# Performance work log

Measured on AMD Instinct MI355X. Metric: run time of the kernel, lower is better.

The kernel has to match this reference:

```python
import jax, jax.numpy as jnp
import numpy as np


def fwht(x):
    """Unnormalized fast Walsh-Hadamard transform over a 1-D vector (len = power of 2).
    Matches the torch chunk/cat stage ordering (MSB-first butterfly)."""
    n = x.shape[0]
    ll = int(round(np.log2(n)))
    for ii in range(ll):
        x = x.reshape(2 ** ii, 2, -1)
        x = jnp.concatenate([x[:, :1] + x[:, 1:], x[:, :1] - x[:, 1:]], axis=1)
    return x.reshape(n)


@jax.custom_vjp
def fwht_ff(x):
    # mirrors torch FastWalshHadamard.apply: plain FWHT forward,
    # backward = FWHT(grad) / sqrt(n) (as defined in the original autograd Function)
    return fwht(x)

def _fwht_ff_fwd(x):
    scale = jnp.asarray(1.0 / np.sqrt(float(x.shape[0])), x.dtype)
    return fwht(x), scale

def _fwht_ff_bwd(scale, g):
    return (scale * fwht(g),)

fwht_ff.defvjp(_fwht_ff_fwd, _fwht_ff_bwd)


def fastfood(theta, BB, Pi, GG, DD):
    """Fastfood projection of theta (dim dd) to DD dims using fixed vars."""
    LL = BB.shape[0]
    dd = theta.shape[0]
    k = min(dd, LL)  # F.pad with negative pad truncates; replicate that
    xx = jnp.zeros(LL, theta.dtype).at[:k].set(theta[:k])
    m2 = fwht(BB * xx)          # H B x
    m4 = m2[Pi] * GG            # G Pi H B x
    m5 = fwht_ff(m4)            # H G Pi H B x
    divisor = jnp.sqrt(LL * jnp.sum(GG * GG))
    return m5[:DD] / (divisor * np.sqrt(float(DD) / LL))


def _mk_ff_vars(key, DD):
    ll = int(np.ceil(np.log2(DD)))
    LL = 2 ** ll
    k1, k2, k3 = jax.random.split(key, 3)
    BB = jax.random.randint(k1, (LL,), 0, 2).astype(jnp.float32) * 2.0 - 1.0
    Pi = jax.random.permutation(k2, LL).astype(jnp.int32)
    GG = jax.random.normal(k3, (LL,), dtype=jnp.float32)
    return BB, Pi, GG


D_IN, D_HID, D_OUT = 768, 3072, 768
INTRINSIC = 2048
BATCH = 256


def setup_inputs() -> dict:
    key = jax.random.key(0)
    ks = jax.random.split(key, 12)
    x = jax.random.normal(ks[0], (BATCH, D_IN), dtype=jnp.float32)
    # original initializes intrinsic_parameter to zeros; use small randn so the
    # Fastfood path contributes non-trivially to the output for testing
    theta = jax.random.normal(ks[1], (INTRINSIC,), dtype=jnp.float32) * 0.01
    init_W1 = jax.random.normal(ks[2], (D_HID, D_IN), dtype=jnp.float32) * 0.02
    init_b1 = jax.random.normal(ks[3], (D_HID,), dtype=jnp.float32) * 0.02
    init_W2 = jax.random.normal(ks[4], (D_OUT, D_HID), dtype=jnp.float32) * 0.02
    init_b2 = jax.random.normal(ks[5], (D_OUT,), dtype=jnp.float32) * 0.02
    BB_W1, Pi_W1, GG_W1 = _mk_ff_vars(ks[6], D_HID * D_IN)
    BB_b1, Pi_b1, GG_b1 = _mk_ff_vars(ks[7], D_HID)
    BB_W2, Pi_W2, GG_W2 = _mk_ff_vars(ks[8], D_OUT * D_HID)
    BB_b2, Pi_b2, GG_b2 = _mk_ff_vars(ks[9], D_OUT)
    return {
        'x': x, 'theta': theta,
        'init_W1': init_W1, 'init_b1': init_b1, 'init_W2': init_W2, 'init_b2': init_b2,
        'BB_W1': BB_W1, 'Pi_W1': Pi_W1, 'GG_W1': GG_W1,
        'BB_b1': BB_b1, 'Pi_b1': Pi_b1, 'GG_b1': GG_b1,
        'BB_W2': BB_W2, 'Pi_W2': Pi_W2, 'GG_W2': GG_W2,
        'BB_b2': BB_b2, 'Pi_b2': Pi_b2, 'GG_b2': GG_b2,
    }


def reference(x, theta, init_W1, init_b1, init_W2, init_b2,
              BB_W1, Pi_W1, GG_W1, BB_b1, Pi_b1, GG_b1,
              BB_W2, Pi_W2, GG_W2, BB_b2, Pi_b2, GG_b2):
    # param = initial_value + fastfood(theta) for every wrapped parameter
    W1 = init_W1 + fastfood(theta, BB_W1, Pi_W1, GG_W1, init_W1.size).reshape(init_W1.shape)
    b1 = init_b1 + fastfood(theta, BB_b1, Pi_b1, GG_b1, init_b1.size)
    W2 = init_W2 + fastfood(theta, BB_W2, Pi_W2, GG_W2, init_W2.size).reshape(init_W2.shape)
    b2 = init_b2 + fastfood(theta, BB_b2, Pi_b2, GG_b2, init_b2.size)
    # wrapped module forward: Linear -> ReLU -> Linear
    h = jax.nn.relu(x @ W1.T + b1)
    return h @ W2.T + b2
```

## Files before the change

### kernel.cpp

```cpp
#include <hip/hip_runtime.h>
#include <hip/hip_bf16.h>

typedef __attribute__((ext_vector_type(8))) short bf16x8;
typedef __attribute__((ext_vector_type(8))) unsigned short u16x8;
typedef __attribute__((ext_vector_type(4))) float f32x4;

#define LLW 4194304

template <int N, int S>
__device__ __forceinline__ void reg_fwht(float* v) {
#pragma unroll
  for (int h = 1; h < N; h <<= 1)
#pragma unroll
    for (int g = 0; g < N; g += 2 * h)
#pragma unroll
      for (int j = 0; j < h; ++j) {
        float a = v[(g + j) * S], b = v[(g + j + h) * S];
        v[(g + j) * S] = a + b;
        v[(g + j + h) * S] = a - b;
      }
}

__device__ __forceinline__ unsigned short f2bf(float f) {
  unsigned u = __float_as_uint(f);
  unsigned r = (u + 0x7fff + ((u >> 16) & 1)) >> 16;
  return (unsigned short)r;
}

__device__ __forceinline__ void lds_fwht(float* s, int n, int tid, int T) {
  for (int h = 1; h < n; h <<= 1) {
    __syncthreads();
    for (int t = tid; t < (n >> 1); t += T) {
      int i0 = ((t & ~(h - 1)) << 1) | (t & (h - 1));
      int i1 = i0 + h;
      float a = s[i0], b = s[i1];
      s[i0] = a + b;
      s[i1] = a - b;
    }
  }
  __syncthreads();
}

__device__ __forceinline__ void fwht2048_block(float w[8], float* pad,
                                               float* dst, int t) {
  reg_fwht<8, 1>(w);
#pragma unroll
  for (int j = 0; j < 8; ++j) {
    int i = t + 256 * j;
    pad[i + 4 * (i >> 5)] = w[j];
  }
  __syncthreads();
  {
    int base = 8 * t + 4 * (t >> 2);
    float4 a = *(float4*)(pad + base);
    float4 b = *(float4*)(pad + base + 4);
    float u[8] = {a.x, a.y, a.z, a.w, b.x, b.y, b.z, b.w};
    reg_fwht<8, 1>(u);
    *(float4*)(pad + base) = make_float4(u[0], u[1], u[2], u[3]);
    *(float4*)(pad + base + 4) = make_float4(u[4], u[5], u[6], u[7]);
  }
  __syncthreads();
  {
    int b0 = (t & 7) + 64 * (t >> 3);
    float u[8];
#pragma unroll
    for (int j = 0; j < 8; ++j) {
      int i = b0 + 8 * j;
      u[j] = pad[i + 4 * (i >> 5)];
    }
    reg_fwht<8, 1>(u);
#pragma unroll
    for (int j = 0; j < 8; ++j) {
      int i = b0 + 8 * j;
      pad[i + 4 * (i >> 5)] = u[j];
    }
  }
  __syncthreads();
#pragma unroll
  for (int g = 0; g < 2; ++g) {
    int b0 = (t & 63) + 256 * ((g << 2) | (t >> 6));
    float u[4];
#pragma unroll
    for (int j = 0; j < 4; ++j) {
      int i = b0 + 64 * j;
      u[j] = pad[i + 4 * (i >> 5)];
    }
    reg_fwht<4, 1>(u);
#pragma unroll
    for (int j = 0; j < 4; ++j) dst[b0 + 64 * j] = u[j];
  }
  __syncthreads();
}

__global__ __launch_bounds__(256, 4) void k_front(
    const float* __restrict__ BB1, const int* __restrict__ Pi1,
    const float* __restrict__ GG1, const float* __restrict__ BB2,
    const int* __restrict__ Pi2, const float* __restrict__ GG2,
    unsigned short* __restrict__ m4b, float* __restrict__ partial,
    const float* __restrict__ theta, const float* __restrict__ BBb1,
    const int* __restrict__ Pib1, const float* __restrict__ GGb1,
    const float* __restrict__ ib1, float* __restrict__ b1w,
    const float* __restrict__ BBb2, const int* __restrict__ Pib2,
    const float* __restrict__ GGb2, const float* __restrict__ ib2,
    float* __restrict__ b2w, const float* __restrict__ x,
    __hip_bfloat16* __restrict__ xb) {
  __shared__ __align__(16) float s[9216];
  __shared__ float red[4];
  int b = blockIdx.x, t = threadIdx.x;

  if (b >= 98) {
    int job = b - 98;
    int pipe = job >> 9, chunk = job & 511;
    const float* BB = pipe ? BB2 : BB1;
    const int* Pi = pipe ? Pi2 : Pi1;
    const float* GG = pipe ? GG2 : GG1;

    long base = (long)chunk * 8192;
    const int4* p4 = (const int4*)(Pi + base);
    const float4* g4 = (const float4*)(GG + base);
    int4 pp[8];
    float4 gg[8];
#pragma unroll
    for (int j = 0; j < 8; ++j) {
      pp[j] = p4[t + j * 256];
      gg[j] = g4[t + j * 256];
    }

    {
      float w8[8];
#pragma unroll
      for (int j = 0; j < 8; ++j) {
        int i = t + 256 * j;
        w8[j] = BB[i] * theta[i];
      }
      fwht2048_block(w8, s + 2304, s, t);
    }

    float v[32];
    float lsum = 0.f;
#pragma unroll
    for (int j = 0; j < 8; ++j) {
      lsum += gg[j].x * gg[j].x + gg[j].y * gg[j].y + gg[j].z * gg[j].z +
              gg[j].w * gg[j].w;
      v[j * 4 + 0] = s[pp[j].x & 2047] * gg[j].x;
      v[j * 4 + 1] = s[pp[j].y & 2047] * gg[j].y;
      v[j * 4 + 2] = s[pp[j].z & 2047] * gg[j].z;
      v[j * 4 + 3] = s[pp[j].w & 2047] * gg[j].w;
    }
    for (int off = 32; off; off >>= 1) lsum += __shfl_down(lsum, off, 64);
    if ((t & 63) == 0) red[t >> 6] = lsum;

#pragma unroll
    for (int e = 0; e < 4; ++e) reg_fwht<8, 4>(v + e);

    __syncthreads();
    if (t == 0)
      partial[pipe * 512 + chunk] = red[0] + red[1] + red[2] + red[3];

#pragma unroll
    for (int j = 0; j < 8; ++j) {
      int A = t * 4 + 4 * (t >> 3) + j * 1152;
      *(float4*)(s + A) =
          make_float4(v[j * 4], v[j * 4 + 1], v[j * 4 + 2], v[j * 4 + 3]);
    }
    __syncthreads();
    {
      int b0 = (t & 31) + (t >> 5) * 1024;
      float w[32];
#pragma unroll
      for (int j2 = 0; j2 < 32; ++j2) {
        int i = b0 + j2 * 32;
        w[j2] = s[i + 4 * (i >> 5)];
      }
      reg_fwht<32, 1>(w);
#pragma unroll
      for (int j2 = 0; j2 < 32; ++j2) {
        int i = b0 + j2 * 32;
        s[i + 4 * (i >> 5)] = w[j2];
      }
    }
    __syncthreads();
#pragma unroll
    for (int q = 0; q < 8; ++q) {
      float4 r = *(const float4*)(s + t * 36 + q * 4);
      v[q * 4 + 0] = r.x;
      v[q * 4 + 1] = r.y;
      v[q * 4 + 2] = r.z;
      v[q * 4 + 3] = r.w;
    }
    reg_fwht<32, 1>(v);
    unsigned short* o = m4b + (long)pipe * LLW;
    long a0 = (long)(2 * t) * 8192 + (long)chunk * 16;
#pragma unroll
    for (int q = 0; q < 4; ++q) {
      u16x8 pk;
#pragma unroll
      for (int e = 0; e < 8; ++e) pk[e] = f2bf(v[q * 8 + e]);
      *(u16x8*)(o + a0 + (q >> 1) * 8192 + (q & 1) * 8) = pk;
    }
  } else if (b < 96) {
    int id0 = b * 256 + t;
#pragma unroll
    for (int it = 0; it < 2; ++it) {
      int id = id0 + it * 24576;
      float4 xv = ((const float4*)x)[id];
      ushort4 o;
      o.x = f2bf(xv.x);
      o.y = f2bf(xv.y);
      o.z = f2bf(xv.z);
      o.w = f2bf(xv.w);
      ((ushort4*)xb)[id] = o;
    }
  } else if (b == 96) {
    float* tabd = s + 6144;
    float w[8];
#pragma unroll
    for (int j = 0; j < 8; ++j) {
      int i = t + 256 * j;
      w[j] = BBb1[i] * theta[i];
    }
    fwht2048_block(w, s, tabd, t);

    float w16[16];
    float lsum = 0.f;
#pragma unroll
    for (int j = 0; j < 16; ++j) {
      int i = t + 256 * j;
      float g = GGb1[i];
      lsum += g * g;
      w16[j] = tabd[Pib1[i] & 2047] * g;
    }
    reg_fwht<16, 1>(w16);
#pragma unroll
    for (int j = 0; j < 16; ++j) {
      int i = t + 256 * j;
      s[i + 4 * (i >> 5)] = w16[j];
    }
    for (int off = 32; off; off >>= 1) lsum += __shfl_down(lsum, off, 64);
    if ((t & 63) == 0) s[4608 + (t >> 6)] = lsum;
    __syncthreads();
    float S = s[4608] + s[4609] + s[4610] + s[4611];
    {
      int base16 = 16 * t + 4 * (t >> 1);
      float u[16];
#pragma unroll
      for (int q = 0; q < 4; ++q) {
        float4 r = *(float4*)(s + base16 + q * 4);
        u[q * 4 + 0] = r.x;
        u[q * 4 + 1] = r.y;
        u[q * 4 + 2] = r.z;
        u[q * 4 + 3] = r.w;
      }
      reg_fwht<16, 1>(u);
#pragma unroll
      for (int q = 0; q < 4; ++q)
        *(float4*)(s + base16 + q * 4) =
            make_float4(u[q * 4], u[q * 4 + 1], u[q * 4 + 2], u[q * 4 + 3]);
    }
    __syncthreads();
    {
      float scale = 1.0f / sqrtf(S * 3072.0f);
      int b0 = (t & 15) + 256 * (t >> 4);
      float u[16];
#pragma unroll
      for (int j = 0; j < 16; ++j) {
        int i = b0 + 16 * j;
        u[j] = s[i + 4 * (i >> 5)];
      }
      reg_fwht<16, 1>(u);
#pragma unroll
      for (int j = 0; j < 16; ++j) {
        int i = b0 + 16 * j;
        if (i < 3072) b1w[i] = ib1[i] + u[j] * scale;
      }
    }
  } else {
    float* tab2 = s;
    float* m42 = s + 1024;
    for (int i = t; i < 1024; i += 256) tab2[i] = BBb2[i] * theta[i];
    lds_fwht(tab2, 1024, t, 256);
    float lsum = 0.f;
    for (int i = t; i < 1024; i += 256) {
      float g = GGb2[i];
      lsum += g * g;
      m42[i] = tab2[Pib2[i] & 1023] * g;
    }
    for (int off = 32; off; off >>= 1) lsum += __shfl_down(lsum, off, 64);
    if ((t & 63) == 0) s[2048 + (t >> 6)] = lsum;
    lds_fwht(m42, 1024, t, 256);
    float S = s[2048] + s[2049] + s[2050] + s[2051];
    float scale = 1.0f / sqrtf(S * 768.0f);
    for (int i = t; i < 768; i += 256) b2w[i] = ib2[i] + m42[i] * scale;
  }
}

__global__ __launch_bounds__(256) void k_f2c(
    const unsigned short* __restrict__ m4b, const float* __restrict__ iW1,
    const float* __restrict__ iW2, const float* __restrict__ partial,
    __hip_bfloat16* __restrict__ W1b, __hip_bfloat16* __restrict__ W2b) {
  __shared__ __align__(16) float s[10480];
  __shared__ float red[4];
  int b = blockIdx.x, t = threadIdx.x;
  int pipe = b >> 9;
  int lb = b & 511;
  int g = ((lb & 7) << 6) | (lb >> 3);
  int l0 = g * 16;
  const unsigned short* mp = m4b + (long)pipe * LLW + (long)g * 8192;
  const float* initW = pipe ? iW2 : iW1;
  unsigned short* outW = (unsigned short*)(pipe ? W2b : W1b);

  float4 ivp[5];
#pragma unroll
  for (int u = 0; u < 5; ++u) {
    int idx = t + u * 256;
    if (idx < 1152) {
      int r = idx >> 2, c4 = (idx & 3) * 4;
      ivp[u] = *(const float4*)(initW + (long)r * 8192 + l0 + c4);
    }
  }

  {
    float ps = partial[pipe * 512 + t] + partial[pipe * 512 + 256 + t];
    for (int off = 32; off; off >>= 1) ps += __shfl_down(ps, off, 64);
    if ((t & 63) == 0) red[t >> 6] = ps;
  }

#pragma unroll
  for (int q = 0; q < 4; ++q) {
    u16x8 raw = *(const u16x8*)(mp + t * 32 + q * 8);
    int r = 2 * t + (q >> 1), cb = (q & 1) * 8;
    float* dp = s + r * 20 + (r >> 5) * 16 + cb;
    float4 f0, f1v;
    f0.x = __uint_as_float((unsigned)raw[0] << 16);
    f0.y = __uint_as_float((unsigned)raw[1] << 16);
    f0.z = __uint_as_float((unsigned)raw[2] << 16);
    f0.w = __uint_as_float((unsigned)raw[3] << 16);
    f1v.x = __uint_as_float((unsigned)raw[4] << 16);
    f1v.y = __uint_as_float((unsigned)raw[5] << 16);
    f1v.z = __uint_as_float((unsigned)raw[6] << 16);
    f1v.w = __uint_as_float((unsigned)raw[7] << 16);
    *(float4*)dp = f0;
    *(float4*)(dp + 4) = f1v;
  }
  __syncthreads();

  {
    int c = t & 15, rg = t >> 4;
    float w[32];
#pragma unroll
    for (int j = 0; j < 32; ++j) {
      int r = rg * 32 + j;
      w[j] = s[r * 20 + (r >> 5) * 16 + c];
    }
    reg_fwht<32, 1>(w);
#pragma unroll
    for (int j = 0; j < 32; ++j) {
      int r = rg * 32 + j;
      s[r * 20 + (r >> 5) * 16 + c] = w[j];
    }
  }
  __syncthreads();

  {
    int c = t & 15;
    float w[32];
#pragma unroll
    for (int k = 0; k < 2; ++k) {
      int b0 = (t >> 4) * 2 + k;
#pragma unroll
      for (int j4 = 0; j4 < 16; ++j4) {
        int r = b0 + 32 * j4;
        w[k * 16 + j4] = s[r * 20 + (r >> 5) * 16 + c];
      }
      reg_fwht<16, 1>(w + k * 16);
#pragma unroll
      for (int j4 = 0; j4 < 16; ++j4) {
        int r = b0 + 32 * j4;
        s[r * 20 + (r >> 5) * 16 + c] = w[k * 16 + j4];
      }
    }
  }
  __syncthreads();

  float S = red[0] + red[1] + red[2] + red[3];
  float scale = 1.0f / sqrtf(S * 2359296.0f);
#pragma unroll
  for (int u = 0; u < 5; ++u) {
    int idx = t + u * 256;
    if (idx < 1152) {
      int r = idx >> 2, c4 = (idx & 3) * 4;
      const float* sp = s + r * 20 + (r >> 5) * 16 + c4;
      long gi = (long)r * 8192 + l0 + c4;
      ushort4 pk;
      pk.x = f2bf(ivp[u].x + sp[0] * scale);
      pk.y = f2bf(ivp[u].y + sp[1] * scale);
      pk.z = f2bf(ivp[u].z + sp[2] * scale);
      pk.w = f2bf(ivp[u].w + sp[3] * scale);
      *(ushort4*)(outW + gi) = pk;
    }
  }
}

template <int NACC, int SPLITK, bool RELU, bool OUT_BF16>
__global__ __launch_bounds__(256) void k_gemm(
    const __hip_bfloat16* __restrict__ A, const __hip_bfloat16* __restrict__ B,
    const float* __restrict__ bias, void* __restrict__ C, int M, int N, int K) {
  __shared__ float red[4 * NACC * 320];
  int wave = threadIdx.x >> 6, lane = threadIdx.x & 63;
  int tileid = blockIdx.x * (4 / SPLITK) + wave / SPLITK;
  int sk = wave % SPLITK;
  int ntiles = N / (16 * NACC);
  int mt = tileid / ntiles, nt = tileid % ntiles;
  int ml = lane & 15;
  int q = lane >> 4;
  const short* As = (const short*)A;
  const short* Bs = (const short*)B;
  long arow = (long)(mt * 16 + ml) * K + q * 8;
  int KS = K / SPLITK, k0 = sk * KS;
  f32x4 acc[NACC] = {};
  for (int k = k0; k < k0 + KS; k += 32) {
    bf16x8 av = *(const bf16x8*)(As + arow + k);
#pragma unroll
    for (int a = 0; a < NACC; ++a) {
      int n = nt * 16 * NACC + a * 16 + ml;
      bf16x8 bv = *(const bf16x8*)(Bs + (long)n * K + q * 8 + k);
      acc[a] = __builtin_amdgcn_mfma_f32_16x16x32_bf16(av, bv, acc[a], 0, 0, 0);
    }
  }
#pragma unroll
  for (int a = 0; a < NACC; ++a)
#pragma unroll
    for (int r = 0; r < 4; ++r)
      red[(wave * NACC + a) * 320 + lane * 5 + r] = acc[a][r];
  __syncthreads();
  if (sk == 0) {
#pragma unroll
    for (int a = 0; a < NACC; ++a) {
      int n = nt * 16 * NACC + a * 16 + ml;
      float bv = bias[n];
#pragma unroll
      for (int r = 0; r < 4; ++r) {
        float vv = bv;
#pragma unroll
        for (int j = 0; j < SPLITK; ++j)
          vv += red[((wave + j) * NACC + a) * 320 + lane * 5 + r];
        int mm = mt * 16 + q * 4 + r;
        if (RELU) vv = fmaxf(vv, 0.f);
        if (OUT_BF16)
          ((__hip_bfloat16*)C)[(long)mm * N + n] = __float2bfloat16(vv);
        else
          ((float*)C)[(long)mm * N + n] = vv;
      }
    }
  }
}

#define OFF_PART 0
#define OFF_M2S 4096
#define OFF_M4B (OFF_M2S + 16384)
#define OFF_W1B (OFF_M4B + 2 * LLW * 2)
#define OFF_W2B (OFF_W1B + 4718592)
#define OFF_HB (OFF_W2B + 4718592)
#define OFF_XB (OFF_HB + 1572864)
#define OFF_B1 (OFF_XB + 393216)
#define OFF_B2 (OFF_B1 + 12288)

extern "C" void kernel_launch(void* const* d_in, const int* in_sizes, int n_in,
                              void* d_out, int out_size, void* d_ws,
                              size_t ws_size, hipStream_t stream) {
  const float* x = (const float*)d_in[0];
  const float* theta = (const float*)d_in[1];
  const float* iW1 = (const float*)d_in[2];
  const float* ib1 = (const float*)d_in[3];
  const float* iW2 = (const float*)d_in[4];
  const float* ib2 = (const float*)d_in[5];
  const float* BB_W1 = (const float*)d_in[6];
  const int* Pi_W1 = (const int*)d_in[7];
  const float* GG_W1 = (const float*)d_in[8];
  const float* BB_b1 = (const float*)d_in[9];
  const int* Pi_b1 = (const int*)d_in[10];
  const float* GG_b1 = (const float*)d_in[11];
  const float* BB_W2 = (const float*)d_in[12];
  const int* Pi_W2 = (const int*)d_in[13];
  const float* GG_W2 = (const float*)d_in[14];
  const float* BB_b2 = (const float*)d_in[15];
  const int* Pi_b2 = (const int*)d_in[16];
  const float* GG_b2 = (const float*)d_in[17];

  char* ws = (char*)d_ws;
  float* partial = (float*)(ws + OFF_PART);
  unsigned short* m4b = (unsigned short*)(ws + OFF_M4B);
  __hip_bfloat16* W1b = (__hip_bfloat16*)(ws + OFF_W1B);
  __hip_bfloat16* W2b = (__hip_bfloat16*)(ws + OFF_W2B);
  __hip_bfloat16* hb = (__hip_bfloat16*)(ws + OFF_HB);
  __hip_bfloat16* xb = (__hip_bfloat16*)(ws + OFF_XB);
  float* b1w = (float*)(ws + OFF_B1);
  float* b2w = (float*)(ws + OFF_B2);

  k_front<<<1122, 256, 0, stream>>>(BB_W1, Pi_W1, GG_W1, BB_W2, Pi_W2, GG_W2,
                                    m4b, partial, theta, BB_b1, Pi_b1, GG_b1,
                                    ib1, b1w, BB_b2, Pi_b2, GG_b2, ib2, b2w, x,
                                    xb);
  k_f2c<<<1024, 256, 0, stream>>>(m4b, iW1, iW2, partial, W1b, W2b);
  k_gemm<2, 2, true, true><<<768, 256, 0, stream>>>(xb, W1b, b1w, hb, 256,
                                                    3072, 768);
  k_gemm<1, 4, false, false><<<768, 256, 0, stream>>>(hb, W2b, b2w, d_out, 256,
                                                      768, 3072);
}
```

Baseline: 215.3 us.

## Run front Fastfood kernel with 512-thread blocks and re-stage 8192-point FWHT

Raises the k_front block size from 256 to 512 threads. Each thread now holds 16 elements of the 8192-point transform instead of 32. The transform after the permutation is rebuilt as a 4-point register stage, two 16-point LDS stages and an 8-point stage fused into the bf16 store. The aim is to cut register pressure and raise occupancy and parallelism per chunk. In exchange, the 2048-point theta transform uses only half the threads, and the deeper staging adds an extra LDS round trip and barrier.

```diff
diff --git a/kernel.cpp b/kernel.cpp
--- a/kernel.cpp
+++ b/kernel.cpp
@@ -41,16 +41,18 @@
   __syncthreads();
 }
 
-__device__ __forceinline__ void fwht2048_block(float w[8], float* pad,
-                                               float* dst, int t) {
-  reg_fwht<8, 1>(w);
-#pragma unroll
-  for (int j = 0; j < 8; ++j) {
-    int i = t + 256 * j;
-    pad[i + 4 * (i >> 5)] = w[j];
-  }
-  __syncthreads();
-  {
+__device__ __forceinline__ void fwht2048_block_g(float w[8], float* pad,
+                                                 float* dst, int t, bool act) {
+  if (act) {
+    reg_fwht<8, 1>(w);
+#pragma unroll
+    for (int j = 0; j < 8; ++j) {
+      int i = t + 256 * j;
+      pad[i + 4 * (i >> 5)] = w[j];
+    }
+  }
+  __syncthreads();
+  if (act) {
     int base = 8 * t + 4 * (t >> 2);
     float4 a = *(float4*)(pad + base);
     float4 b = *(float4*)(pad + base + 4);
@@ -60,7 +62,7 @@
     *(float4*)(pad + base + 4) = make_float4(u[4], u[5], u[6], u[7]);
   }
   __syncthreads();
-  {
+  if (act) {
     int b0 = (t & 7) + 64 * (t >> 3);
     float u[8];
 #pragma unroll
@@ -76,23 +78,25 @@
     }
   }
   __syncthreads();
-#pragma unroll
-  for (int g = 0; g < 2; ++g) {
-    int b0 = (t & 63) + 256 * ((g << 2) | (t >> 6));
-    float u[4];
-#pragma unroll
-    for (int j = 0; j < 4; ++j) {
-      int i = b0 + 64 * j;
-      u[j] = pad[i + 4 * (i >> 5)];
-    }
-    reg_fwht<4, 1>(u);
-#pragma unroll
-    for (int j = 0; j < 4; ++j) dst[b0 + 64 * j] = u[j];
-  }
-  __syncthreads();
-}
-
-__global__ __launch_bounds__(256, 4) void k_front(
+  if (act) {
+#pragma unroll
+    for (int g = 0; g < 2; ++g) {
+      int b0 = (t & 63) + 256 * ((g << 2) | (t >> 6));
+      float u[4];
+#pragma unroll
+      for (int j = 0; j < 4; ++j) {
+        int i = b0 + 64 * j;
+        u[j] = pad[i + 4 * (i >> 5)];
+      }
+      reg_fwht<4, 1>(u);
+#pragma unroll
+      for (int j = 0; j < 4; ++j) dst[b0 + 64 * j] = u[j];
+    }
+  }
+  __syncthreads();
+}
+
+__global__ __launch_bounds__(512, 6) void k_front(
     const float* __restrict__ BB1, const int* __restrict__ Pi1,
     const float* __restrict__ GG1, const float* __restrict__ BB2,
     const int* __restrict__ Pi2, const float* __restrict__ GG2,
@@ -105,7 +109,7 @@
     float* __restrict__ b2w, const float* __restrict__ x,
     __hip_bfloat16* __restrict__ xb) {
   __shared__ __align__(16) float s[9216];
-  __shared__ float red[4];
+  __shared__ float red[8];
   int b = blockIdx.x, t = threadIdx.x;
 
   if (b >= 98) {
@@ -118,28 +122,31 @@
     long base = (long)chunk * 8192;
     const int4* p4 = (const int4*)(Pi + base);
     const float4* g4 = (const float4*)(GG + base);
-    int4 pp[8];
-    float4 gg[8];
-#pragma unroll
-    for (int j = 0; j < 8; ++j) {
-      pp[j] = p4[t + j * 256];
-      gg[j] = g4[t + j * 256];
+    int4 pp[4];
+    float4 gg[4];
+#pragma unroll
+    for (int j = 0; j < 4; ++j) {
+      pp[j] = p4[t + j * 512];
+      gg[j] = g4[t + j * 512];
     }
 
     {
+      bool act = t < 256;
       float w8[8];
-#pragma unroll
-      for (int j = 0; j < 8; ++j) {
-        int i = t + 256 * j;
-        w8[j] = BB[i] * theta[i];
-      }
-      fwht2048_block(w8, s + 2304, s, t);
-    }
-
-    float v[32];
+      if (act) {
+#pragma unroll
+        for (int j = 0; j < 8; ++j) {
+          int i = t + 256 * j;
+          w8[j] = BB[i] * theta[i];
+        }
+      }
+      fwht2048_block_g(w8, s + 2304, s, t, act);
+    }
+
+    float v[16];
     float lsum = 0.f;
 #pragma unroll
-    for (int j = 0; j < 8; ++j) {
+    for (int j = 0; j < 4; ++j) {
       lsum += gg[j].x * gg[j].x + gg[j].y * gg[j].y + gg[j].z * gg[j].z +
               gg[j].w * gg[j].w;
       v[j * 4 + 0] = s[pp[j].x & 2047] * gg[j].x;
@@ -151,96 +158,115 @@
     if ((t & 63) == 0) red[t >> 6] = lsum;
 
 #pragma unroll
-    for (int e = 0; e < 4; ++e) reg_fwht<8, 4>(v + e);
-
-    __syncthreads();
-    if (t == 0)
-      partial[pipe * 512 + chunk] = red[0] + red[1] + red[2] + red[3];
-
-#pragma unroll
-    for (int j = 0; j < 8; ++j) {
-      int A = t * 4 + 4 * (t >> 3) + j * 1152;
+    for (int e = 0; e < 4; ++e) reg_fwht<4, 4>(v + e);
+
+    __syncthreads();
+    if (t == 0) {
+      float S = 0.f;
+#pragma unroll
+      for (int i = 0; i < 8; ++i) S += red[i];
+      partial[pipe * 512 + chunk] = S;
+    }
+
+#pragma unroll
+    for (int j = 0; j < 4; ++j) {
+      int A = 4 * t + 4 * (t >> 3) + 2304 * j;
       *(float4*)(s + A) =
           make_float4(v[j * 4], v[j * 4 + 1], v[j * 4 + 2], v[j * 4 + 3]);
     }
     __syncthreads();
     {
-      int b0 = (t & 31) + (t >> 5) * 1024;
-      float w[32];
-#pragma unroll
-      for (int j2 = 0; j2 < 32; ++j2) {
-        int i = b0 + j2 * 32;
-        w[j2] = s[i + 4 * (i >> 5)];
-      }
-      reg_fwht<32, 1>(w);
-#pragma unroll
-      for (int j2 = 0; j2 < 32; ++j2) {
-        int i = b0 + j2 * 32;
-        s[i + 4 * (i >> 5)] = w[j2];
-      }
-    }
-    __syncthreads();
-#pragma unroll
-    for (int q = 0; q < 8; ++q) {
-      float4 r = *(const float4*)(s + t * 36 + q * 4);
-      v[q * 4 + 0] = r.x;
-      v[q * 4 + 1] = r.y;
-      v[q * 4 + 2] = r.z;
-      v[q * 4 + 3] = r.w;
-    }
-    reg_fwht<32, 1>(v);
+      int low7 = t & 127, hi2 = t >> 7;
+      float w[16];
+#pragma unroll
+      for (int k = 0; k < 16; ++k) {
+        int i = low7 + 128 * k + 2048 * hi2;
+        w[k] = s[i + 4 * (i >> 5)];
+      }
+      reg_fwht<16, 1>(w);
+#pragma unroll
+      for (int k = 0; k < 16; ++k) {
+        int i = low7 + 128 * k + 2048 * hi2;
+        s[i + 4 * (i >> 5)] = w[k];
+      }
+    }
+    __syncthreads();
+    {
+      int low3 = t & 7, hi6 = t >> 3;
+      float w[16];
+#pragma unroll
+      for (int k = 0; k < 16; ++k) {
+        int i = low3 + 8 * k + 128 * hi6;
+        w[k] = s[i + 4 * (i >> 5)];
+      }
+      reg_fwht<16, 1>(w);
+#pragma unroll
+      for (int k = 0; k < 16; ++k) {
+        int i = low3 + 8 * k + 128 * hi6;
+        s[i + 4 * (i >> 5)] = w[k];
+      }
+    }
+    __syncthreads();
     unsigned short* o = m4b + (long)pipe * LLW;
-    long a0 = (long)(2 * t) * 8192 + (long)chunk * 16;
-#pragma unroll
-    for (int q = 0; q < 4; ++q) {
+#pragma unroll
+    for (int g = 0; g < 2; ++g) {
+      int hi10 = t + 512 * g;
+      int i0 = 8 * hi10;
+      int A = i0 + 4 * (i0 >> 5);
+      float4 a = *(const float4*)(s + A);
+      float4 c4 = *(const float4*)(s + A + 4);
+      float u[8] = {a.x, a.y, a.z, a.w, c4.x, c4.y, c4.z, c4.w};
+      reg_fwht<8, 1>(u);
       u16x8 pk;
 #pragma unroll
-      for (int e = 0; e < 8; ++e) pk[e] = f2bf(v[q * 8 + e]);
-      *(u16x8*)(o + a0 + (q >> 1) * 8192 + (q & 1) * 8) = pk;
+      for (int e = 0; e < 8; ++e) pk[e] = f2bf(u[e]);
+      long addr = (long)(hi10 >> 1) * 8192 + (long)chunk * 16 + (hi10 & 1) * 8;
+      *(u16x8*)(o + addr) = pk;
     }
   } else if (b < 96) {
-    int id0 = b * 256 + t;
-#pragma unroll
-    for (int it = 0; it < 2; ++it) {
-      int id = id0 + it * 24576;
-      float4 xv = ((const float4*)x)[id];
-      ushort4 o;
-      o.x = f2bf(xv.x);
-      o.y = f2bf(xv.y);
-      o.z = f2bf(xv.z);
-      o.w = f2bf(xv.w);
-      ((ushort4*)xb)[id] = o;
-    }
+    int id = b * 512 + t;
+    float4 xv = ((const float4*)x)[id];
+    ushort4 ov;
+    ov.x = f2bf(xv.x);
+    ov.y = f2bf(xv.y);
+    ov.z = f2bf(xv.z);
+    ov.w = f2bf(xv.w);
+    ((ushort4*)xb)[id] = ov;
   } else if (b == 96) {
+    bool act = t < 256;
     float* tabd = s + 6144;
     float w[8];
-#pragma unroll
-    for (int j = 0; j < 8; ++j) {
-      int i = t + 256 * j;
-      w[j] = BBb1[i] * theta[i];
-    }
-    fwht2048_block(w, s, tabd, t);
+    if (act) {
+#pragma unroll
+      for (int j = 0; j < 8; ++j) {
+        int i = t + 256 * j;
+        w[j] = BBb1[i] * theta[i];
+      }
+    }
+    fwht2048_block_g(w, s, tabd, t, act);
 
     float w16[16];
     float lsum = 0.f;
-#pragma unroll
-    for (int j = 0; j < 16; ++j) {
-      int i = t + 256 * j;
-      float g = GGb1[i];
-      lsum += g * g;
-      w16[j] = tabd[Pib1[i] & 2047] * g;
-    }
-    reg_fwht<16, 1>(w16);
-#pragma unroll
-    for (int j = 0; j < 16; ++j) {
-      int i = t + 256 * j;
-      s[i + 4 * (i >> 5)] = w16[j];
-    }
-    for (int off = 32; off; off >>= 1) lsum += __shfl_down(lsum, off, 64);
-    if ((t & 63) == 0) s[4608 + (t >> 6)] = lsum;
+    if (act) {
+#pragma unroll
+      for (int j = 0; j < 16; ++j) {
+        int i = t + 256 * j;
+        float g = GGb1[i];
+        lsum += g * g;
+        w16[j] = tabd[Pib1[i] & 2047] * g;
+      }
+      reg_fwht<16, 1>(w16);
+#pragma unroll
+      for (int j = 0; j < 16; ++j) {
+        int i = t + 256 * j;
+        s[i + 4 * (i >> 5)] = w16[j];
+      }
+      for (int off = 32; off; off >>= 1) lsum += __shfl_down(lsum, off, 64);
+      if ((t & 63) == 0) s[4608 + (t >> 6)] = lsum;
+    }
     __syncthreads();
     float S = s[4608] + s[4609] + s[4610] + s[4611];
-    {
+    if (act) {
       int base16 = 16 * t + 4 * (t >> 1);
       float u[16];
 #pragma unroll
@@ -258,7 +284,7 @@
             make_float4(u[q * 4], u[q * 4 + 1], u[q * 4 + 2], u[q * 4 + 3]);
     }
     __syncthreads();
-    {
+    if (act) {
       float scale = 1.0f / sqrtf(S * 3072.0f);
       int b0 = (t & 15) + 256 * (t >> 4);
       float u[16];
@@ -277,20 +303,22 @@
   } else {
     float* tab2 = s;
     float* m42 = s + 1024;
-    for (int i = t; i < 1024; i += 256) tab2[i] = BBb2[i] * theta[i];
-    lds_fwht(tab2, 1024, t, 256);
+    for (int i = t; i < 1024; i += 512) tab2[i] = BBb2[i] * theta[i];
+    lds_fwht(tab2, 1024, t, 512);
     float lsum = 0.f;
-    for (int i = t; i < 1024; i += 256) {
+    for (int i = t; i < 1024; i += 512) {
       float g = GGb2[i];
       lsum += g * g;
       m42[i] = tab2[Pib2[i] & 1023] * g;
     }
     for (int off = 32; off; off >>= 1) lsum += __shfl_down(lsum, off, 64);
     if ((t & 63) == 0) s[2048 + (t >> 6)] = lsum;
-    lds_fwht(m42, 1024, t, 256);
-    float S = s[2048] + s[2049] + s[2050] + s[2051];
+    lds_fwht(m42, 1024, t, 512);
+    float S = 0.f;
+#pragma unroll
+    for (int i = 0; i < 8; ++i) S += s[2048 + i];
     float scale = 1.0f / sqrtf(S * 768.0f);
-    for (int i = t; i < 768; i += 256) b2w[i] = ib2[i] + m42[i] * scale;
+    for (int i = t; i < 768; i += 512) b2w[i] = ib2[i] + m42[i] * scale;
   }
 }
 
@@ -497,7 +525,7 @@
   float* b1w = (float*)(ws + OFF_B1);
   float* b2w = (float*)(ws + OFF_B2);
 
-  k_front<<<1122, 256, 0, stream>>>(BB_W1, Pi_W1, GG_W1, BB_W2, Pi_W2, GG_W2,
+  k_front<<<1122, 512, 0, stream>>>(BB_W1, Pi_W1, GG_W1, BB_W2, Pi_W2, GG_W2,
                                     m4b, partial, theta, BB_b1, Pi_b1, GG_b1,
                                     ib1, b1w, BB_b2, Pi_b2, GG_b2, ib2, b2w, x,
                                     xb);
```

Measured after the change: 213.0 us. About the same (-1.1%).
